# Kernel optimization log

Hardware: AMD Instinct MI355X
Metric: run time of the kernel (lower is better)

## Reference

```python
import jax, jax.numpy as jnp
import numpy as np

B, C, D, H, W = 1, 32, 48, 64, 208
EPS = 1e-5  # BatchNorm eps


def setup_inputs() -> dict:
    key = jax.random.key(0)
    ks = jax.random.split(key, 8)
    x = jax.random.normal(ks[0], (B, C, D, H, W), jnp.float32)
    g = jax.random.normal(ks[1], (B, 20, H, W), jnp.float32)
    conv_w = jax.random.normal(ks[2], (C, C, 3, 3, 3), jnp.float32) * 0.02
    bn1_gamma = 1.0 + 0.1 * jax.random.normal(ks[3], (C,), jnp.float32)
    bn1_beta = 0.1 * jax.random.normal(ks[4], (C,), jnp.float32)
    bn1_mean = 0.1 * jax.random.normal(ks[5], (C,), jnp.float32)
    bn1_var = jax.random.uniform(ks[6], (C,), jnp.float32, 0.5, 1.5)
    bn2_gamma = 1.0 + 0.1 * jax.random.normal(ks[7], (C,), jnp.float32)
    bn2_beta = jnp.zeros((C,), jnp.float32)
    bn2_mean = jnp.zeros((C,), jnp.float32)
    bn2_var = jnp.ones((C,), jnp.float32)
    return {
        'x': x, 'g': g, 'conv_w': conv_w,
        'bn1_gamma': bn1_gamma, 'bn1_beta': bn1_beta, 'bn1_mean': bn1_mean, 'bn1_var': bn1_var,
        'bn2_gamma': bn2_gamma, 'bn2_beta': bn2_beta, 'bn2_mean': bn2_mean, 'bn2_var': bn2_var,
    }


def _l1_normalize(k):
    # F.normalize(k, p=1, dim=1)
    return k / jnp.maximum(jnp.sum(jnp.abs(k), axis=1, keepdims=True), 1e-12)


def _sga_scan(x, w):
    """Directional semi-global aggregation along the LAST axis.
    x: [B,C,D,H,L] cost volume, w: [B,5,H,L] L1-normalized guidance weights.
    Recurrence (GANet SGA):
      A[p,d] = w0*x[p,d] + w1*A[p-1,d] + w2*A[p-1,d-1] + w3*A[p-1,d+1] + w4*max_d' A[p-1,d']
    """
    xs = jnp.moveaxis(x, -1, 0)  # [L,B,C,D,H]
    ws = jnp.moveaxis(w, -1, 0)  # [L,B,5,H]

    def step(prev, inp):
        xi, wi = inp  # [B,C,D,H], [B,5,H]
        w0, w1, w2, w3, w4 = [wi[:, i][:, None, None, :] for i in range(5)]
        up = jnp.concatenate([prev[:, :, :1], prev[:, :, :-1]], axis=2)   # A[d-1]
        dn = jnp.concatenate([prev[:, :, 1:], prev[:, :, -1:]], axis=2)   # A[d+1]
        mx = jnp.max(prev, axis=2, keepdims=True)                          # max_d A
        out = w0 * xi + w1 * prev + w2 * up + w3 * dn + w4 * mx
        return out, out

    _, outs = jax.lax.scan(step, xs[0], (xs, ws))  # boundary: carry init = raw cost slice
    return jnp.moveaxis(outs, 0, -1)


def _sga(x, k1, k2, k3, k4):
    # direction 1: left -> right (along W)
    d1 = _sga_scan(x, k1)
    # direction 2: right -> left
    d2 = jnp.flip(_sga_scan(jnp.flip(x, -1), jnp.flip(k2, -1)), -1)
    # vertical directions: swap H<->W so the scan axis is H
    xv = jnp.swapaxes(x, 3, 4)  # [B,C,D,W,H]
    d3 = jnp.swapaxes(_sga_scan(xv, jnp.swapaxes(k3, 2, 3)), 3, 4)  # top -> bottom
    d4 = jnp.swapaxes(
        jnp.flip(_sga_scan(jnp.flip(xv, -1), jnp.flip(jnp.swapaxes(k4, 2, 3), -1)), -1), 3, 4)
    # GANet combines directions with an elementwise max
    return jnp.maximum(jnp.maximum(d1, d2), jnp.maximum(d3, d4))


def _bn3d(x, gamma, beta, mean, var):
    s = (gamma / jnp.sqrt(var + EPS))[None, :, None, None, None]
    return (x - mean[None, :, None, None, None]) * s + beta[None, :, None, None, None]


def _conv3d_same(x, w):
    return jax.lax.conv_general_dilated(
        x, w, window_strides=(1, 1, 1), padding=[(1, 1)] * 3,
        dimension_numbers=('NCDHW', 'OIDHW', 'NCDHW'))


def reference(x, g, conv_w, bn1_gamma, bn1_beta, bn1_mean, bn1_var,
              bn2_gamma, bn2_beta, bn2_mean, bn2_var):
    rem = x
    k1, k2, k3, k4 = jnp.split(g, 4, axis=1)  # each [B,5,H,W]
    k1, k2, k3, k4 = map(_l1_normalize, (k1, k2, k3, k4))
    a = _sga(x, k1, k2, k3, k4)
    # refine=True branch: BN+ReLU then BasicConv(3x3x3, BN, no relu)
    a = jax.nn.relu(_bn3d(a, bn1_gamma, bn1_beta, bn1_mean, bn1_var))
    a = _conv3d_same(a, conv_w)
    a = _bn3d(a, bn2_gamma, bn2_beta, bn2_mean, bn2_var)
    return jax.nn.relu(a + rem)
```

## Files before the change

kernel.cpp:

```cpp
#include <hip/hip_runtime.h>
#include <hip/hip_bf16.h>
#include <cstddef>

#define C_ 32
#define D_ 48
#define H_ 64
#define W_ 208
#define HW_ 13312
#define HS_ 9984
#define EPS_ 1e-5f

typedef __attribute__((ext_vector_type(8))) short short8;
typedef __attribute__((ext_vector_type(4))) float float4v;
typedef __attribute__((ext_vector_type(16))) float float16v;

template<int CTRL>
__device__ __forceinline__ float dppmov(float x) {
    int v = __builtin_bit_cast(int, x);
    return __builtin_bit_cast(float,
        __builtin_amdgcn_update_dpp(v, v, CTRL, 0xf, 0xf, false));
}
template<int CTRL>
__device__ __forceinline__ float dppmax(float m) {
    return fmaxf(m, dppmov<CTRL>(m));
}
__device__ __forceinline__ float rl(float v, int idx) {
    return __builtin_bit_cast(float,
        __builtin_amdgcn_readlane(__builtin_bit_cast(int, v), idx));
}

__device__ __forceinline__ float sga_step_dpp(float A, float xi,
    float w0, float w1, float w2, float w3, float w4, bool actv, bool ge47)
{
    float up = dppmov<0x138>(A);
    float dn = dppmov<0x130>(A);
    dn = ge47 ? A : dn;
    float m = actv ? A : -3.4e38f;
    m = dppmax<0x111>(m);
    m = dppmax<0x112>(m);
    m = dppmax<0x114>(m);
    m = dppmax<0x118>(m);
    m = dppmax<0x142>(m);
    m = dppmax<0x143>(m);
    float mall = rl(m, 63);
    return (w0*xi + w1*A) + ((w2*up + w3*dn) + w4*mall);
}

__global__ __launch_bounds__(256) void prep_kernel(
    const float* __restrict__ g, const float* __restrict__ cw,
    float* __restrict__ wn, float* __restrict__ wnT,
    __hip_bfloat16* __restrict__ wrep)
{
    int idx = blockIdx.x * 256 + threadIdx.x;
    if (idx < 4 * HW_) {
        int dir = idx / HW_;
        int hw  = idx % HW_;
        const float* gb = g + dir * 5 * HW_ + hw;
        float v0 = gb[0*HW_], v1 = gb[1*HW_], v2 = gb[2*HW_], v3 = gb[3*HW_], v4 = gb[4*HW_];
        float s = fabsf(v0)+fabsf(v1)+fabsf(v2)+fabsf(v3)+fabsf(v4);
        float inv = 1.0f / fmaxf(s, 1e-12f);
        v0 *= inv; v1 *= inv; v2 *= inv; v3 *= inv; v4 *= inv;
        float* ob = wn + dir * 5 * HW_ + hw;
        ob[0*HW_] = v0; ob[1*HW_] = v1; ob[2*HW_] = v2; ob[3*HW_] = v3; ob[4*HW_] = v4;
        if (dir >= 2) {
            int hq = hw / W_, wq = hw % W_;
            float* oT = wnT + ((size_t)((dir-2)*5)*W_ + wq)*H_ + hq;
            oT[0]       = v0; oT[1*HW_] = v1; oT[2*HW_] = v2;
            oT[3*HW_]   = v3; oT[4*HW_] = v4;
        }
    } else {
        int j = idx - 4 * HW_;
        if (j < 27 * 2 * 64 * 8) {
            int e    = j & 7;
            int lane = (j >> 3) & 63;
            int q    = j >> 9;
            int cih  = q & 1;
            int tap  = q >> 1;
            int co = lane & 31;
            int ci = cih * 16 + (lane >> 5) * 8 + e;
            wrep[j] = __float2bfloat16(cw[(co * C_ + ci) * 27 + tap]);
        }
    }
}

__global__ __launch_bounds__(256) void t0_kernel(
    const float* __restrict__ x, float* __restrict__ xt)
{
    __shared__ float t[48 * 257];
    int tid = threadIdx.x;
    int c  = blockIdx.x / 52;
    int q0 = (blockIdx.x % 52) * 256;
    #pragma unroll
    for (int dd = 0; dd < 48; ++dd)
        t[dd * 257 + tid] = x[((size_t)c * 48 + dd) * HW_ + q0 + tid];
    __syncthreads();
    #pragma unroll
    for (int k = 0; k < 48; ++k) {
        int f = tid + 256 * k;
        int dd = f % 48, hwl = f / 48;
        xt[((size_t)c * HW_ + q0 + hwl) * 48 + dd] = t[dd * 257 + hwl];
    }
}

template<int LN>
__device__ __forceinline__ float chunk_fwd(float A,
    const float* __restrict__ xp, __hip_bfloat16* __restrict__ dp,
    const float* __restrict__ wb, int P0, int lane, bool actv, bool ge47)
{
    float xr[LN];
    #pragma unroll
    for (int j = 0; j < LN; ++j) xr[j] = xp[(size_t)(P0 + j) * 48];
    int lm = lane & (LN - 1);
    float wv0 = wb[0*HW_ + P0 + lm], wv1 = wb[1*HW_ + P0 + lm],
          wv2 = wb[2*HW_ + P0 + lm], wv3 = wb[3*HW_ + P0 + lm],
          wv4 = wb[4*HW_ + P0 + lm];
    #pragma unroll
    for (int j = 0; j < LN; ++j) {
        A = sga_step_dpp(A, xr[j], rl(wv0,j), rl(wv1,j), rl(wv2,j),
                         rl(wv3,j), rl(wv4,j), actv, ge47);
        if (actv) dp[(size_t)(P0 + j) * 48] = __float2bfloat16(A);
    }
    return A;
}

template<int LN>
__device__ __forceinline__ float chunk_rev(float A,
    const float* __restrict__ xp, __hip_bfloat16* __restrict__ dp,
    const float* __restrict__ wb, int P0, int lane, bool actv, bool ge47)
{
    float xr[LN]; __hip_bfloat16 dr[LN];
    #pragma unroll
    for (int j = 0; j < LN; ++j) {
        xr[j] = xp[(size_t)(P0 + j) * 48];
        dr[j] = dp[(size_t)(P0 + j) * 48];
    }
    int lm = lane & (LN - 1);
    float wv0 = wb[0*HW_ + P0 + lm], wv1 = wb[1*HW_ + P0 + lm],
          wv2 = wb[2*HW_ + P0 + lm], wv3 = wb[3*HW_ + P0 + lm],
          wv4 = wb[4*HW_ + P0 + lm];
    #pragma unroll
    for (int j = LN - 1; j >= 0; --j) {
        A = sga_step_dpp(A, xr[j], rl(wv0,j), rl(wv1,j), rl(wv2,j),
                         rl(wv3,j), rl(wv4,j), actv, ge47);
        if (actv)
            dp[(size_t)(P0 + j) * 48] =
                __float2bfloat16(fmaxf(__bfloat162float(dr[j]), A));
    }
    return A;
}

__global__ __launch_bounds__(256) void sga_w_kernel(
    const float* __restrict__ xt, const float* __restrict__ wn,
    __hip_bfloat16* __restrict__ d12)
{
    int lane = threadIdx.x & 63;
    int wid  = blockIdx.x * 4 + (threadIdx.x >> 6);
    int c = wid >> 6, h = wid & 63;
    int d = lane < 48 ? lane : 47;
    bool actv = lane < 48, ge47 = lane >= 47;
    const float* xp = xt + ((size_t)c * HW_ + h * W_) * 48 + d;
    __hip_bfloat16* dp = d12 + ((size_t)c * HW_ + h * W_) * 48 + d;
    const float* w1 = wn + (size_t)0 * 5 * HW_ + h * W_;
    const float* w2 = wn + (size_t)1 * 5 * HW_ + h * W_;

    float A = xp[0];
    for (int cc = 0; cc < 6; ++cc)
        A = chunk_fwd<32>(A, xp, dp, w1, cc * 32, lane, actv, ge47);
    A = chunk_fwd<16>(A, xp, dp, w1, 192, lane, actv, ge47);

    A = xp[(size_t)207 * 48];
    A = chunk_rev<16>(A, xp, dp, w2, 192, lane, actv, ge47);
    for (int cc = 0; cc < 6; ++cc)
        A = chunk_rev<32>(A, xp, dp, w2, 160 - cc * 32, lane, actv, ge47);
}

__global__ __launch_bounds__(256) void sga_h_kernel(
    const float* __restrict__ xt, const float* __restrict__ wnT,
    __hip_bfloat16* __restrict__ d12,
    const float* __restrict__ g1, const float* __restrict__ b1,
    const float* __restrict__ m1, const float* __restrict__ v1)
{
    int lane = threadIdx.x & 63;
    int wid  = blockIdx.x * 4 + (threadIdx.x >> 6);
    int c = wid / W_, w = wid % W_;
    int d = lane < 48 ? lane : 47;
    bool actv = lane < 48, ge47 = lane >= 47;
    const float* xp = xt + ((size_t)c * HW_ + w) * 48 + d;
    __hip_bfloat16* dp = d12 + ((size_t)c * HW_ + w) * 48 + d;
    const float* w3 = wnT + ((size_t)0 * W_ + w) * H_;
    const float* w4 = wnT + ((size_t)5 * W_ + w) * H_;

    float s1 = g1[c] * rsqrtf(v1[c] + EPS_);
    float o1 = b1[c] - m1[c] * s1;

    float d3v[64];
    float A = xp[0];
    #pragma unroll
    for (int cc = 0; cc < 4; ++cc) {
        int h0 = cc * 16;
        float xr[16];
        #pragma unroll
        for (int j = 0; j < 16; ++j) xr[j] = xp[(size_t)(h0 + j) * HS_];
        int lm = lane & 15;
        float wv0 = w3[0*HW_ + h0 + lm], wv1 = w3[1*HW_ + h0 + lm],
              wv2 = w3[2*HW_ + h0 + lm], wv3 = w3[3*HW_ + h0 + lm],
              wv4 = w3[4*HW_ + h0 + lm];
        #pragma unroll
        for (int j = 0; j < 16; ++j) {
            A = sga_step_dpp(A, xr[j], rl(wv0,j), rl(wv1,j), rl(wv2,j),
                             rl(wv3,j), rl(wv4,j), actv, ge47);
            d3v[h0 + j] = A;
        }
    }
    A = xp[(size_t)63 * HS_];
    #pragma unroll
    for (int cc = 0; cc < 4; ++cc) {
        int h0 = 48 - cc * 16;
        float xr[16]; __hip_bfloat16 dr[16];
        #pragma unroll
        for (int j = 0; j < 16; ++j) {
            xr[j] = xp[(size_t)(h0 + j) * HS_];
            dr[j] = dp[(size_t)(h0 + j) * HS_];
        }
        int lm = lane & 15;
        float wv0 = w4[0*HW_ + h0 + lm], wv1 = w4[1*HW_ + h0 + lm],
              wv2 = w4[2*HW_ + h0 + lm], wv3 = w4[3*HW_ + h0 + lm],
              wv4 = w4[4*HW_ + h0 + lm];
        #pragma unroll
        for (int j = 15; j >= 0; --j) {
            A = sga_step_dpp(A, xr[j], rl(wv0,j), rl(wv1,j), rl(wv2,j),
                             rl(wv3,j), rl(wv4,j), actv, ge47);
            if (actv) {
                float comb = fmaxf(fmaxf(d3v[h0 + j], A), __bfloat162float(dr[j]));
                dp[(size_t)(h0 + j) * HS_] =
                    __float2bfloat16(fmaxf(comb * s1 + o1, 0.0f));
            }
        }
    }
}

__global__ __launch_bounds__(256) void trans_kernel(
    const __hip_bfloat16* __restrict__ st, __hip_bfloat16* __restrict__ act)
{
    __shared__ float t[8 * 1571];
    int tid = threadIdx.x;
    int h  = blockIdx.x / 26;
    int w0 = (blockIdx.x % 26) * 8;
    const unsigned* stu = (const unsigned*)st;
    #pragma unroll
    for (int k = 0; k < 24; ++k) {
        int f = tid + 256 * k;
        int d2 = f % 24, wl = (f / 24) % 8, c = f / 192;
        unsigned u = stu[(((size_t)c * HW_ + h * W_ + w0 + wl) * 48 + 2 * d2) >> 1];
        const __hip_bfloat16* bp = (const __hip_bfloat16*)&u;
        t[wl * 1571 + c * 49 + 2 * d2]     = __bfloat162float(bp[0]);
        t[wl * 1571 + c * 49 + 2 * d2 + 1] = __bfloat162float(bp[1]);
    }
    __syncthreads();
    unsigned* actu = (unsigned*)act;
    #pragma unroll
    for (int k = 0; k < 24; ++k) {
        int f = tid + 256 * k;
        int cp = f % 16, wl = (f / 16) % 8, d = f / 128;
        union { unsigned u; __hip_bfloat16 hh[2]; } pk;
        pk.hh[0] = __float2bfloat16(t[wl * 1571 + (2 * cp) * 49 + d]);
        pk.hh[1] = __float2bfloat16(t[wl * 1571 + (2 * cp + 1) * 49 + d]);
        actu[(((size_t)h * 48 + d) * W_ + w0 + wl) * 16 + cp] = pk.u;
    }
}

__global__ __launch_bounds__(256) void conv_kernel(
    const __hip_bfloat16* __restrict__ act,
    const short8* __restrict__ wrep,
    const float* __restrict__ x,
    const float* __restrict__ g2, const float* __restrict__ b2,
    const float* __restrict__ m2, const float* __restrict__ v2,
    float* __restrict__ out)
{
    int lane = threadIdx.x & 63;
    int wid  = blockIdx.x * 4 + (threadIdx.x >> 6);
    int wt = wid % 7;
    int t1 = wid / 7;
    int h  = t1 & 63;
    int d0 = (t1 >> 6) * 4;
    int w0 = wt * 32;
    int n   = lane & 31;
    int ci0 = (lane >> 5) * 8;

    float16v acc[4];
    #pragma unroll
    for (int i = 0; i < 4; ++i) acc[i] = (float16v)(0.0f);

    #pragma unroll
    for (int kh = 0; kh < 3; ++kh) {
        int hh = h + kh - 1;
        if (hh < 0 || hh >= H_) continue;
        #pragma unroll
        for (int kw = 0; kw < 3; ++kw) {
            int ww = w0 + kw - 1 + n;
            bool wok = (ww >= 0 && ww < W_);
            int wwc = wok ? ww : 0;
            const __hip_bfloat16* pl = act + ((size_t)hh * D_ * W_ + wwc) * C_;
            #pragma unroll
            for (int cih = 0; cih < 2; ++cih) {
                short8 af[3];
                #pragma unroll
                for (int kd = 0; kd < 3; ++kd)
                    af[kd] = wrep[(((kd*3 + kh)*3 + kw)*2 + cih)*64 + lane];
                #pragma unroll
                for (int p = 0; p < 6; ++p) {
                    int dd = d0 - 1 + p;
                    if (dd < 0 || dd >= D_) continue;
                    short8 bf = {0,0,0,0,0,0,0,0};
                    if (wok)
                        bf = *(const short8*)(pl + (size_t)dd * W_ * C_ + cih*16 + ci0);
                    #pragma unroll
                    for (int kd = 0; kd < 3; ++kd) {
                        int pi = p - kd;
                        if (pi < 0 || pi > 3) continue;
                        acc[pi] = __builtin_amdgcn_mfma_f32_32x32x16_bf16(
                            af[kd], bf, acc[pi], 0, 0, 0);
                    }
                }
            }
        }
    }

    int wl = w0 + n;
    bool wvalid = wl < W_;
    int coh = 4 * (lane >> 5);
    #pragma unroll
    for (int r = 0; r < 16; ++r) {
        int co = (r & 3) + 8 * (r >> 2) + coh;
        float s2 = g2[co] * rsqrtf(v2[co] + EPS_);
        float o2 = b2[co] - m2[co] * s2;
        #pragma unroll
        for (int pi = 0; pi < 4; ++pi) {
            size_t idx = ((size_t)(co * D_ + d0 + pi) * H_ + h) * W_ + wl;
            if (wvalid)
                out[idx] = fmaxf(acc[pi][r] * s2 + o2 + x[idx], 0.0f);
        }
    }
}

extern "C" void kernel_launch(void* const* d_in, const int* in_sizes, int n_in,
                              void* d_out, int out_size, void* d_ws, size_t ws_size,
                              hipStream_t stream)
{
    const float* x    = (const float*)d_in[0];
    const float* g    = (const float*)d_in[1];
    const float* cw   = (const float*)d_in[2];
    const float* bn1g = (const float*)d_in[3];
    const float* bn1b = (const float*)d_in[4];
    const float* bn1m = (const float*)d_in[5];
    const float* bn1v = (const float*)d_in[6];
    const float* bn2g = (const float*)d_in[7];
    const float* bn2b = (const float*)d_in[8];
    const float* bn2m = (const float*)d_in[9];
    const float* bn2v = (const float*)d_in[10];
    float* out = (float*)d_out;

    char* ws = (char*)d_ws;
    float* wn  = (float*)ws;
    float* wnT = (float*)(ws + 1064960);
    __hip_bfloat16* wrep = (__hip_bfloat16*)(ws + 1597440);
    __hip_bfloat16* d12t = (__hip_bfloat16*)(ws + 1652736);
    __hip_bfloat16* act  = (__hip_bfloat16*)(ws + 42547200);
    float* xt = out;

    prep_kernel<<<316, 256, 0, stream>>>(g, cw, wn, wnT, wrep);
    t0_kernel<<<1664, 256, 0, stream>>>(x, xt);
    sga_w_kernel<<<512, 256, 0, stream>>>(xt, wn, d12t);
    sga_h_kernel<<<1664, 256, 0, stream>>>(xt, wnT, d12t, bn1g, bn1b, bn1m, bn1v);
    trans_kernel<<<1664, 256, 0, stream>>>(d12t, act);
    conv_kernel<<<1344, 256, 0, stream>>>(act, (const short8*)wrep, x,
                                          bn2g, bn2b, bn2m, bn2v, out);
}
```

Measured before the change: 449.2 us.

## Store transposed cost volume in bf16 and halve conv depth tile per wave

The transposed input volume that both SGA scan kernels read is now written and read as bf16 instead of fp32. This halves the memory traffic of the transpose and the scans, at the cost of rounding the raw cost input before aggregation. Separately, the conv kernel now computes 2 depth slices per wave instead of 4, with twice as many blocks and a launch_bounds occupancy hint. That lowers register pressure and raises parallelism, but it reloads more overlapping depth rows per output.

```diff
diff --git a/kernel.cpp b/kernel.cpp
--- a/kernel.cpp
+++ b/kernel.cpp
@@ -84,7 +84,7 @@
 }
 
 __global__ __launch_bounds__(256) void t0_kernel(
-    const float* __restrict__ x, float* __restrict__ xt)
+    const float* __restrict__ x, __hip_bfloat16* __restrict__ xt)
 {
     __shared__ float t[48 * 257];
     int tid = threadIdx.x;
@@ -94,22 +94,26 @@
     for (int dd = 0; dd < 48; ++dd)
         t[dd * 257 + tid] = x[((size_t)c * 48 + dd) * HW_ + q0 + tid];
     __syncthreads();
-    #pragma unroll
-    for (int k = 0; k < 48; ++k) {
+    unsigned* xtu = (unsigned*)xt;
+    #pragma unroll
+    for (int k = 0; k < 24; ++k) {
         int f = tid + 256 * k;
-        int dd = f % 48, hwl = f / 48;
-        xt[((size_t)c * HW_ + q0 + hwl) * 48 + dd] = t[dd * 257 + hwl];
+        int d2 = f % 24, hwl = f / 24;
+        union { unsigned u; __hip_bfloat16 hh[2]; } pk;
+        pk.hh[0] = __float2bfloat16(t[(2 * d2) * 257 + hwl]);
+        pk.hh[1] = __float2bfloat16(t[(2 * d2 + 1) * 257 + hwl]);
+        xtu[(((size_t)c * HW_ + q0 + hwl) * 48 + 2 * d2) >> 1] = pk.u;
     }
 }
 
 template<int LN>
 __device__ __forceinline__ float chunk_fwd(float A,
-    const float* __restrict__ xp, __hip_bfloat16* __restrict__ dp,
+    const __hip_bfloat16* __restrict__ xp, __hip_bfloat16* __restrict__ dp,
     const float* __restrict__ wb, int P0, int lane, bool actv, bool ge47)
 {
     float xr[LN];
     #pragma unroll
-    for (int j = 0; j < LN; ++j) xr[j] = xp[(size_t)(P0 + j) * 48];
+    for (int j = 0; j < LN; ++j) xr[j] = __bfloat162float(xp[(size_t)(P0 + j) * 48]);
     int lm = lane & (LN - 1);
     float wv0 = wb[0*HW_ + P0 + lm], wv1 = wb[1*HW_ + P0 + lm],
           wv2 = wb[2*HW_ + P0 + lm], wv3 = wb[3*HW_ + P0 + lm],
@@ -125,13 +129,13 @@
 
 template<int LN>
 __device__ __forceinline__ float chunk_rev(float A,
-    const float* __restrict__ xp, __hip_bfloat16* __restrict__ dp,
+    const __hip_bfloat16* __restrict__ xp, __hip_bfloat16* __restrict__ dp,
     const float* __restrict__ wb, int P0, int lane, bool actv, bool ge47)
 {
     float xr[LN]; __hip_bfloat16 dr[LN];
     #pragma unroll
     for (int j = 0; j < LN; ++j) {
-        xr[j] = xp[(size_t)(P0 + j) * 48];
+        xr[j] = __bfloat162float(xp[(size_t)(P0 + j) * 48]);
         dr[j] = dp[(size_t)(P0 + j) * 48];
     }
     int lm = lane & (LN - 1);
@@ -150,7 +154,7 @@
 }
 
 __global__ __launch_bounds__(256) void sga_w_kernel(
-    const float* __restrict__ xt, const float* __restrict__ wn,
+    const __hip_bfloat16* __restrict__ xt, const float* __restrict__ wn,
     __hip_bfloat16* __restrict__ d12)
 {
     int lane = threadIdx.x & 63;
@@ -158,24 +162,24 @@
     int c = wid >> 6, h = wid & 63;
     int d = lane < 48 ? lane : 47;
     bool actv = lane < 48, ge47 = lane >= 47;
-    const float* xp = xt + ((size_t)c * HW_ + h * W_) * 48 + d;
+    const __hip_bfloat16* xp = xt + ((size_t)c * HW_ + h * W_) * 48 + d;
     __hip_bfloat16* dp = d12 + ((size_t)c * HW_ + h * W_) * 48 + d;
     const float* w1 = wn + (size_t)0 * 5 * HW_ + h * W_;
     const float* w2 = wn + (size_t)1 * 5 * HW_ + h * W_;
 
-    float A = xp[0];
+    float A = __bfloat162float(xp[0]);
     for (int cc = 0; cc < 6; ++cc)
         A = chunk_fwd<32>(A, xp, dp, w1, cc * 32, lane, actv, ge47);
     A = chunk_fwd<16>(A, xp, dp, w1, 192, lane, actv, ge47);
 
-    A = xp[(size_t)207 * 48];
+    A = __bfloat162float(xp[(size_t)207 * 48]);
     A = chunk_rev<16>(A, xp, dp, w2, 192, lane, actv, ge47);
     for (int cc = 0; cc < 6; ++cc)
         A = chunk_rev<32>(A, xp, dp, w2, 160 - cc * 32, lane, actv, ge47);
 }
 
 __global__ __launch_bounds__(256) void sga_h_kernel(
-    const float* __restrict__ xt, const float* __restrict__ wnT,
+    const __hip_bfloat16* __restrict__ xt, const float* __restrict__ wnT,
     __hip_bfloat16* __restrict__ d12,
     const float* __restrict__ g1, const float* __restrict__ b1,
     const float* __restrict__ m1, const float* __restrict__ v1)
@@ -185,7 +189,7 @@
     int c = wid / W_, w = wid % W_;
     int d = lane < 48 ? lane : 47;
     bool actv = lane < 48, ge47 = lane >= 47;
-    const float* xp = xt + ((size_t)c * HW_ + w) * 48 + d;
+    const __hip_bfloat16* xp = xt + ((size_t)c * HW_ + w) * 48 + d;
     __hip_bfloat16* dp = d12 + ((size_t)c * HW_ + w) * 48 + d;
     const float* w3 = wnT + ((size_t)0 * W_ + w) * H_;
     const float* w4 = wnT + ((size_t)5 * W_ + w) * H_;
@@ -194,13 +198,14 @@
     float o1 = b1[c] - m1[c] * s1;
 
     float d3v[64];
-    float A = xp[0];
+    float A = __bfloat162float(xp[0]);
     #pragma unroll
     for (int cc = 0; cc < 4; ++cc) {
         int h0 = cc * 16;
         float xr[16];
         #pragma unroll
-        for (int j = 0; j < 16; ++j) xr[j] = xp[(size_t)(h0 + j) * HS_];
+        for (int j = 0; j < 16; ++j)
+            xr[j] = __bfloat162float(xp[(size_t)(h0 + j) * HS_]);
         int lm = lane & 15;
         float wv0 = w3[0*HW_ + h0 + lm], wv1 = w3[1*HW_ + h0 + lm],
               wv2 = w3[2*HW_ + h0 + lm], wv3 = w3[3*HW_ + h0 + lm],
@@ -212,14 +217,14 @@
             d3v[h0 + j] = A;
         }
     }
-    A = xp[(size_t)63 * HS_];
+    A = __bfloat162float(xp[(size_t)63 * HS_]);
     #pragma unroll
     for (int cc = 0; cc < 4; ++cc) {
         int h0 = 48 - cc * 16;
         float xr[16]; __hip_bfloat16 dr[16];
         #pragma unroll
         for (int j = 0; j < 16; ++j) {
-            xr[j] = xp[(size_t)(h0 + j) * HS_];
+            xr[j] = __bfloat162float(xp[(size_t)(h0 + j) * HS_]);
             dr[j] = dp[(size_t)(h0 + j) * HS_];
         }
         int lm = lane & 15;
@@ -269,7 +274,7 @@
     }
 }
 
-__global__ __launch_bounds__(256) void conv_kernel(
+__global__ __launch_bounds__(256, 4) void conv_kernel(
     const __hip_bfloat16* __restrict__ act,
     const short8* __restrict__ wrep,
     const float* __restrict__ x,
@@ -282,14 +287,13 @@
     int wt = wid % 7;
     int t1 = wid / 7;
     int h  = t1 & 63;
-    int d0 = (t1 >> 6) * 4;
+    int d0 = (t1 >> 6) * 2;
     int w0 = wt * 32;
     int n   = lane & 31;
     int ci0 = (lane >> 5) * 8;
 
-    float16v acc[4];
-    #pragma unroll
-    for (int i = 0; i < 4; ++i) acc[i] = (float16v)(0.0f);
+    float16v acc0 = (float16v)(0.0f);
+    float16v acc1 = (float16v)(0.0f);
 
     #pragma unroll
     for (int kh = 0; kh < 3; ++kh) {
@@ -300,28 +304,30 @@
             int ww = w0 + kw - 1 + n;
             bool wok = (ww >= 0 && ww < W_);
             int wwc = wok ? ww : 0;
-            const __hip_bfloat16* pl = act + ((size_t)hh * D_ * W_ + wwc) * C_;
+            const __hip_bfloat16* pl =
+                act + ((size_t)hh * D_ * W_ + wwc) * C_ + ci0;
             #pragma unroll
             for (int cih = 0; cih < 2; ++cih) {
+                const __hip_bfloat16* pc = pl + cih * 16;
                 short8 af[3];
                 #pragma unroll
                 for (int kd = 0; kd < 3; ++kd)
                     af[kd] = wrep[(((kd*3 + kh)*3 + kw)*2 + cih)*64 + lane];
+                short8 bf[4];
                 #pragma unroll
-                for (int p = 0; p < 6; ++p) {
+                for (int p = 0; p < 4; ++p) {
                     int dd = d0 - 1 + p;
-                    if (dd < 0 || dd >= D_) continue;
-                    short8 bf = {0,0,0,0,0,0,0,0};
-                    if (wok)
-                        bf = *(const short8*)(pl + (size_t)dd * W_ * C_ + cih*16 + ci0);
-                    #pragma unroll
-                    for (int kd = 0; kd < 3; ++kd) {
-                        int pi = p - kd;
-                        if (pi < 0 || pi > 3) continue;
-                        acc[pi] = __builtin_amdgcn_mfma_f32_32x32x16_bf16(
-                            af[kd], bf, acc[pi], 0, 0, 0);
-                    }
+                    short8 z = {0,0,0,0,0,0,0,0};
+                    bf[p] = z;
+                    if (wok && dd >= 0 && dd < D_)
+                        bf[p] = *(const short8*)(pc + (size_t)dd * W_ * C_);
                 }
+                acc0 = __builtin_amdgcn_mfma_f32_32x32x16_bf16(af[0], bf[0], acc0, 0, 0, 0);
+                acc1 = __builtin_amdgcn_mfma_f32_32x32x16_bf16(af[0], bf[1], acc1, 0, 0, 0);
+                acc0 = __builtin_amdgcn_mfma_f32_32x32x16_bf16(af[1], bf[1], acc0, 0, 0, 0);
+                acc1 = __builtin_amdgcn_mfma_f32_32x32x16_bf16(af[1], bf[2], acc1, 0, 0, 0);
+                acc0 = __builtin_amdgcn_mfma_f32_32x32x16_bf16(af[2], bf[2], acc0, 0, 0, 0);
+                acc1 = __builtin_amdgcn_mfma_f32_32x32x16_bf16(af[2], bf[3], acc1, 0, 0, 0);
             }
         }
     }
@@ -334,11 +340,10 @@
         int co = (r & 3) + 8 * (r >> 2) + coh;
         float s2 = g2[co] * rsqrtf(v2[co] + EPS_);
         float o2 = b2[co] - m2[co] * s2;
-        #pragma unroll
-        for (int pi = 0; pi < 4; ++pi) {
-            size_t idx = ((size_t)(co * D_ + d0 + pi) * H_ + h) * W_ + wl;
-            if (wvalid)
-                out[idx] = fmaxf(acc[pi][r] * s2 + o2 + x[idx], 0.0f);
+        size_t idx0 = ((size_t)(co * D_ + d0) * H_ + h) * W_ + wl;
+        if (wvalid) {
+            out[idx0]       = fmaxf(acc0[r] * s2 + o2 + x[idx0], 0.0f);
+            out[idx0 + HW_] = fmaxf(acc1[r] * s2 + o2 + x[idx0 + HW_], 0.0f);
         }
     }
 }
@@ -366,13 +371,13 @@
     __hip_bfloat16* wrep = (__hip_bfloat16*)(ws + 1597440);
     __hip_bfloat16* d12t = (__hip_bfloat16*)(ws + 1652736);
     __hip_bfloat16* act  = (__hip_bfloat16*)(ws + 42547200);
-    float* xt = out;
+    __hip_bfloat16* xt = (__hip_bfloat16*)out;
 
     prep_kernel<<<316, 256, 0, stream>>>(g, cw, wn, wnT, wrep);
     t0_kernel<<<1664, 256, 0, stream>>>(x, xt);
     sga_w_kernel<<<512, 256, 0, stream>>>(xt, wn, d12t);
     sga_h_kernel<<<1664, 256, 0, stream>>>(xt, wnT, d12t, bn1g, bn1b, bn1m, bn1v);
     trans_kernel<<<1664, 256, 0, stream>>>(d12t, act);
-    conv_kernel<<<1344, 256, 0, stream>>>(act, (const short8*)wrep, x,
+    conv_kernel<<<2688, 256, 0, stream>>>(act, (const short8*)wrep, x,
                                           bn2g, bn2b, bn2m, bn2v, out);
 }
```

New measurement: 432.8 us. 3.6% less time.
